# Kernel tuning notes

Hardware: AMD Instinct MI355X
Metric: run time of the kernel (lower is better)

## Reference

```python
import jax, jax.numpy as jnp
import numpy as np

D_MODEL = 768
N_HEADS = 12
HEAD_DIM = D_MODEL // N_HEADS


def setup_inputs() -> dict:
    key = jax.random.key(0)
    k1, k2, k3 = jax.random.split(key, 3)
    scale = 1.0 / np.sqrt(D_MODEL)
    x = jax.random.normal(k1, (2, 4096, D_MODEL), dtype=jnp.float32)
    W_qkv = jax.random.normal(k2, (D_MODEL, 3 * D_MODEL), dtype=jnp.float32) * scale
    b_qkv = jnp.zeros((3 * D_MODEL,), dtype=jnp.float32)
    W_out = jax.random.normal(k3, (D_MODEL, D_MODEL), dtype=jnp.float32) * scale
    b_out = jnp.zeros((D_MODEL,), dtype=jnp.float32)
    return {"x": x, "W_qkv": W_qkv, "b_qkv": b_qkv, "W_out": W_out, "b_out": b_out}


def reference(x, W_qkv, b_qkv, W_out, b_out):
    B, N, _ = x.shape
    # QKV projection: [B, N, 3*D]
    qkv = x @ W_qkv + b_qkv
    qkv = qkv.reshape(B, N, 3, N_HEADS, HEAD_DIM)
    qkv = jnp.transpose(qkv, (2, 0, 3, 1, 4))  # [3, B, H, N, Dh]
    q, k, v = qkv[0], qkv[1], qkv[2]
    # full NxN score matrix (faithful to the manual implementation)
    score = jnp.einsum('bhqd,bhkd->bhqk', q, k) / np.sqrt(HEAD_DIM).astype(np.float32)
    attn = jax.nn.softmax(score, axis=-1)
    out = jnp.einsum('bhqk,bhkd->bhqd', attn, v)  # [B, H, N, Dh]
    out = jnp.transpose(out, (0, 2, 1, 3)).reshape(B, N, D_MODEL)
    return out @ W_out + b_out
```

## Files before the change

kernel.cpp:

```cpp
#include <hip/hip_runtime.h>

typedef float  f32x4 __attribute__((ext_vector_type(4)));
typedef short  s16x8 __attribute__((ext_vector_type(8)));

__device__ __forceinline__ unsigned short f2bf(float f){
  unsigned int u = __builtin_bit_cast(unsigned int, f);
  return (unsigned short)((u + 0x8000u) >> 16);
}

__device__ __forceinline__ void mfma_bf16(f32x4& c, s16x8 a, s16x8 b){
  asm volatile("v_mfma_f32_16x16x32_bf16 %0, %1, %2, %0" : "+v"(c) : "v"(a), "v"(b));
}

__device__ __forceinline__ void split2(float x, unsigned short& h, unsigned short& l){
  unsigned int u = __builtin_bit_cast(unsigned int, x);
  h = (unsigned short)(u >> 16);
  float hf = __builtin_bit_cast(float, u & 0xFFFF0000u);
  l = (unsigned short)(__builtin_bit_cast(unsigned int, x - hf) >> 16);
}

__device__ __forceinline__ void pack16(const unsigned short* h, uint4& v0, uint4& v1){
  v0.x = h[0] | (h[1] << 16);  v0.y = h[2]  | (h[3] << 16);
  v0.z = h[4] | (h[5] << 16);  v0.w = h[6]  | (h[7] << 16);
  v1.x = h[8] | (h[9] << 16);  v1.y = h[10] | (h[11] << 16);
  v1.z = h[12]| (h[13]<< 16);  v1.w = h[14] | (h[15] << 16);
}

__global__ __launch_bounds__(256) void split_wT(
    const float* __restrict__ W, unsigned short* __restrict__ H,
    unsigned short* __restrict__ L, int N){
  __shared__ float T[64][69];
  const int t = threadIdx.x;
  const int n0 = blockIdx.x * 64, k0 = blockIdx.y * 64;
  {
    int kr = t >> 2, cg = (t & 3) * 16;
    const float* sp = &W[(size_t)(k0 + kr) * N + n0 + cg];
    #pragma unroll
    for (int q = 0; q < 4; ++q)
      *(float4*)&T[kr][cg + q*4] = *(const float4*)(sp + q*4);
  }
  __syncthreads();
  int nr = t >> 2, kg = (t & 3) * 16;
  unsigned short h[16], l[16];
  #pragma unroll
  for (int j = 0; j < 16; ++j) split2(T[kg + j][nr], h[j], l[j]);
  uint4 hv0, hv1, lv0, lv1;
  pack16(h, hv0, hv1);
  pack16(l, lv0, lv1);
  unsigned short* hp = &H[(size_t)(n0 + nr) * 768 + k0 + kg];
  unsigned short* lp = &L[(size_t)(n0 + nr) * 768 + k0 + kg];
  *(uint4*)hp = hv0; *(uint4*)(hp + 8) = hv1;
  *(uint4*)lp = lv0; *(uint4*)(lp + 8) = lv1;
}

__global__ __launch_bounds__(256) void qkv_mfma(
    const float* __restrict__ X,
    const unsigned short* __restrict__ WH, const unsigned short* __restrict__ WL,
    const float* __restrict__ bias, unsigned short* __restrict__ QKV){
  __shared__ __align__(16) char raw[36864];
  char* Abase = raw;
  char* Bbase = raw + 16384;
  const int tid = threadIdx.x;
  const int wave = tid >> 6, lane = tid & 63, r = lane & 15, g = lane >> 4;
  const int wm = wave >> 1, wn = wave & 1;
  const int m0 = blockIdx.y * 128, n0 = blockIdx.x * 128;
  const int srow = tid >> 1, shalf = tid & 1;
  const int sw  = (srow & 7) << 4;
  const int rsw = (r & 7) << 4;

  f32x4 acc[4][4] = {};

  for (int k0 = 0; k0 < 768; k0 += 32){
    const float* ax = &X[(size_t)(m0 + srow) * 768 + k0 + shalf * 16];
    float4 a0 = *(const float4*)ax,     a1 = *(const float4*)(ax + 4);
    float4 a2 = *(const float4*)(ax+8), a3 = *(const float4*)(ax + 12);
    float va[16] = {a0.x,a0.y,a0.z,a0.w, a1.x,a1.y,a1.z,a1.w,
                    a2.x,a2.y,a2.z,a2.w, a3.x,a3.y,a3.z,a3.w};
    unsigned short ah[16], al[16];
    #pragma unroll
    for (int j = 0; j < 16; ++j) split2(va[j], ah[j], al[j]);
    uint4 ah0, ah1, al0, al1;
    pack16(ah, ah0, ah1);
    pack16(al, al0, al1);
    const unsigned short* bwh = &WH[(size_t)(n0 + srow) * 768 + k0 + shalf * 16];
    const unsigned short* bwl = &WL[(size_t)(n0 + srow) * 768 + k0 + shalf * 16];
    uint4 bh0 = *(const uint4*)bwh, bh1 = *(const uint4*)(bwh + 8);
    uint4 bl0 = *(const uint4*)bwl, bl1 = *(const uint4*)(bwl + 8);
    __syncthreads();
    {
      char* ar = Abase + srow * 128;
      *(uint4*)(ar + ((shalf*32     ) ^ sw)) = ah0;
      *(uint4*)(ar + ((shalf*32 + 16) ^ sw)) = ah1;
      *(uint4*)(ar + ((64 + shalf*32     ) ^ sw)) = al0;
      *(uint4*)(ar + ((64 + shalf*32 + 16) ^ sw)) = al1;
      char* br = Bbase + srow * 128;
      *(uint4*)(br + ((shalf*32     ) ^ sw)) = bh0;
      *(uint4*)(br + ((shalf*32 + 16) ^ sw)) = bh1;
      *(uint4*)(br + ((64 + shalf*32     ) ^ sw)) = bl0;
      *(uint4*)(br + ((64 + shalf*32 + 16) ^ sw)) = bl1;
    }
    __syncthreads();
    s16x8 afh[4], afl[4], bfh[4], bfl[4];
    #pragma unroll
    for (int mf = 0; mf < 4; ++mf){
      char* p = Abase + (wm*64 + mf*16 + r) * 128;
      afh[mf] = *(const s16x8*)(p + ((g*16) ^ rsw));
      afl[mf] = *(const s16x8*)(p + ((64 + g*16) ^ rsw));
    }
    #pragma unroll
    for (int nf = 0; nf < 4; ++nf){
      char* p = Bbase + (wn*64 + nf*16 + r) * 128;
      bfh[nf] = *(const s16x8*)(p + ((g*16) ^ rsw));
      bfl[nf] = *(const s16x8*)(p + ((64 + g*16) ^ rsw));
    }
    #pragma unroll
    for (int mf = 0; mf < 4; ++mf)
      #pragma unroll
      for (int nf = 0; nf < 4; ++nf){
        mfma_bf16(acc[mf][nf], afh[mf], bfh[nf]);
        mfma_bf16(acc[mf][nf], afh[mf], bfl[nf]);
        mfma_bf16(acc[mf][nf], afl[mf], bfh[nf]);
      }
  }
  asm volatile("s_nop 7\n\ts_nop 7");
  __syncthreads();

  unsigned short (*ep)[72] = (unsigned short(*)[72])(raw + wave * 9216);
  const int ng0 = n0 + wn * 64;
  const int t3 = ng0 / 768, h = (ng0 % 768) / 64;
  const float sc = (t3 == 0) ? 0.18033688f : 1.0f;
  float bv[4];
  #pragma unroll
  for (int nf = 0; nf < 4; ++nf) bv[nf] = bias[ng0 + nf*16 + r];
  #pragma unroll
  for (int mf = 0; mf < 4; ++mf)
    #pragma unroll
    for (int nf = 0; nf < 4; ++nf)
      #pragma unroll
      for (int t = 0; t < 4; ++t)
        ep[mf*16 + g*4 + t][nf*16 + r] = f2bf((acc[mf][nf][t] + bv[nf]) * sc);
  __syncthreads();

  const int mg0 = m0 + wm * 64;
  const int bb = mg0 >> 12, nr0 = mg0 & 4095;
  unsigned short* dst = QKV + ((size_t)(bb*12 + h)*3 + t3) * 262144;
  if (t3 != 2){
    const int i0 = lane >> 3, ch = lane & 7;
    #pragma unroll
    for (int pass = 0; pass < 8; ++pass){
      int i = pass*8 + i0;
      *(uint4*)&dst[(size_t)(nr0 + i)*64 + ch*8] = *(const uint4*)&ep[i][ch*8];
    }
  } else {
    const int d0 = lane >> 3, kc = lane & 7;
    #pragma unroll
    for (int pass = 0; pass < 8; ++pass){
      int dh = pass*8 + d0;
      unsigned short v[8];
      #pragma unroll
      for (int j = 0; j < 8; ++j) v[j] = ep[kc*8 + j][dh];
      uint4 w;
      w.x = v[0] | (v[1] << 16); w.y = v[2] | (v[3] << 16);
      w.z = v[4] | (v[5] << 16); w.w = v[6] | (v[7] << 16);
      *(uint4*)&dst[(size_t)dh*4096 + nr0 + kc*8] = w;
    }
  }
}

__global__ __launch_bounds__(256, 3) void attn_kernel(
    const unsigned short* __restrict__ QKV, float* __restrict__ AO){
  __shared__ __align__(16) char lds[34816];
  char* Kt = lds;
  char* Vt = lds + 8192;
  const int tid  = threadIdx.x;
  const int wave = tid >> 6, lane = tid & 63;
  const int r = lane & 15, g = lane >> 4;
  const int rsw = (r & 7) << 4;
  unsigned short* pw = (unsigned short*)(lds + 16384 + wave * 4608);
  const int head = blockIdx.x % 24;
  const int qb   = blockIdx.x / 24;
  const size_t base = (size_t)head * 786432;
  const unsigned short* Q  = QKV + base;
  const unsigned short* K  = QKV + base + 262144;
  const unsigned short* VT = QKV + base + 524288;
  const int q0 = qb * 128 + wave * 32;

  s16x8 aq[2][2];
  #pragma unroll
  for (int qs = 0; qs < 2; ++qs){
    const unsigned short* qp = &Q[(size_t)(q0 + qs*16 + r)*64 + g*8];
    aq[qs][0] = *(const s16x8*)qp;
    aq[qs][1] = *(const s16x8*)(qp + 32);
  }

  const int c0 = wave*2, c1 = wave*2 + 1;
  const int srow = lane >> 3;
  const int scol = (lane & 7) * 8;
  const int sgr  = ((lane & 7) ^ srow) * 16;
  const int sdst0 = (c0*8 + srow) * 128 + sgr;
  const int sdst1 = (c1*8 + srow) * 128 + sgr;
  const unsigned short* Kg0 = K  + (size_t)(c0*8 + srow)*64 + scol;
  const unsigned short* Kg1 = K  + (size_t)(c1*8 + srow)*64 + scol;
  const unsigned short* Vg0 = VT + (size_t)(c0*8 + srow)*4096 + scol;
  const unsigned short* Vg1 = VT + (size_t)(c1*8 + srow)*4096 + scol;

  f32x4 o[2][4] = {};
  float lper[2][4] = {};
  uint4 kr0, kr1, vr0, vr1;

  kr0 = *(const uint4*)(Kg0);  kr1 = *(const uint4*)(Kg1);
  vr0 = *(const uint4*)(Vg0);  vr1 = *(const uint4*)(Vg1);
  *(uint4*)(Kt + sdst0) = kr0; *(uint4*)(Kt + sdst1) = kr1;
  *(uint4*)(Vt + sdst0) = vr0; *(uint4*)(Vt + sdst1) = vr1;
  __syncthreads();

  for (int it = 0; it < 64; ++it){
    const int kb = it * 64;
    if (it < 63){
      kr0 = *(const uint4*)(Kg0 + (size_t)(kb + 64)*64);
      kr1 = *(const uint4*)(Kg1 + (size_t)(kb + 64)*64);
      vr0 = *(const uint4*)(Vg0 + kb + 64);
      vr1 = *(const uint4*)(Vg1 + kb + 64);
    }
    f32x4 s[2][4];
    #pragma unroll
    for (int qs = 0; qs < 2; ++qs)
      #pragma unroll
      for (int kh = 0; kh < 4; ++kh) s[qs][kh] = (f32x4){0.f,0.f,0.f,0.f};
    #pragma unroll
    for (int kh = 0; kh < 4; ++kh){
      const char* kp = Kt + (kh*16 + r) * 128;
      s16x8 b0 = *(const s16x8*)(kp + ((g*16) ^ rsw));
      s16x8 b1 = *(const s16x8*)(kp + ((64 + g*16) ^ rsw));
      mfma_bf16(s[0][kh], aq[0][0], b0);
      mfma_bf16(s[0][kh], aq[0][1], b1);
      mfma_bf16(s[1][kh], aq[1][0], b0);
      mfma_bf16(s[1][kh], aq[1][1], b1);
    }
    asm volatile("s_nop 7\n\ts_nop 7");
    __builtin_amdgcn_sched_barrier(0);

    #pragma unroll
    for (int qs = 0; qs < 2; ++qs){
      #pragma unroll
      for (int t = 0; t < 4; ++t){
        float p0 = __builtin_amdgcn_exp2f(s[qs][0][t] - 16.0f);
        float p1 = __builtin_amdgcn_exp2f(s[qs][1][t] - 16.0f);
        float p2 = __builtin_amdgcn_exp2f(s[qs][2][t] - 16.0f);
        float p3 = __builtin_amdgcn_exp2f(s[qs][3][t] - 16.0f);
        lper[qs][t] += (p0 + p1) + (p2 + p3);
        unsigned short* row = pw + (qs*16 + g*4 + t)*72 + r;
        row[0]  = f2bf(p0);
        row[16] = f2bf(p1);
        row[32] = f2bf(p2);
        row[48] = f2bf(p3);
      }
    }

    s16x8 pf[2][2];
    #pragma unroll
    for (int qs = 0; qs < 2; ++qs){
      const unsigned short* pr = pw + (qs*16 + r)*72 + g*8;
      pf[qs][0] = *(const s16x8*)pr;
      pf[qs][1] = *(const s16x8*)(pr + 32);
    }
    #pragma unroll
    for (int dt = 0; dt < 4; ++dt){
      const char* vp = Vt + (dt*16 + r) * 128;
      s16x8 v0 = *(const s16x8*)(vp + ((g*16) ^ rsw));
      s16x8 v1 = *(const s16x8*)(vp + ((64 + g*16) ^ rsw));
      mfma_bf16(o[0][dt], pf[0][0], v0);
      mfma_bf16(o[0][dt], pf[0][1], v1);
      mfma_bf16(o[1][dt], pf[1][0], v0);
      mfma_bf16(o[1][dt], pf[1][1], v1);
    }

    if (it < 63){
      __syncthreads();
      *(uint4*)(Kt + sdst0) = kr0; *(uint4*)(Kt + sdst1) = kr1;
      *(uint4*)(Vt + sdst0) = vr0; *(uint4*)(Vt + sdst1) = vr1;
      __syncthreads();
    }
  }
  asm volatile("s_nop 7\n\ts_nop 7");
  __builtin_amdgcn_sched_barrier(0);

  const int bb = head / 12, h = head % 12;
  #pragma unroll
  for (int qs = 0; qs < 2; ++qs)
    #pragma unroll
    for (int t = 0; t < 4; ++t){
      float l = lper[qs][t];
      l += __shfl_xor(l, 1);
      l += __shfl_xor(l, 2);
      l += __shfl_xor(l, 4);
      l += __shfl_xor(l, 8);
      float inv = 1.0f / l;
      int q = q0 + qs*16 + g*4 + t;
      #pragma unroll
      for (int dt = 0; dt < 4; ++dt)
        AO[(size_t)(bb*4096 + q)*768 + h*64 + dt*16 + r] = o[qs][dt][t] * inv;
    }
}

__global__ __launch_bounds__(256) void out_mfma(
    const float* __restrict__ A,
    const unsigned short* __restrict__ WH, const unsigned short* __restrict__ WL,
    const float* __restrict__ bias, float* __restrict__ OUT){
  __shared__ __align__(16) char raw[32768];
  char* Abase = raw;
  char* Bbase = raw + 16384;
  const int tid = threadIdx.x;
  const int wave = tid >> 6, lane = tid & 63, r = lane & 15, g = lane >> 4;
  const int wm = wave >> 1, wn = wave & 1;
  const int m0 = blockIdx.y * 128, n0 = blockIdx.x * 128;
  const int srow = tid >> 1, shalf = tid & 1;
  const int sw  = (srow & 7) << 4;
  const int rsw = (r & 7) << 4;

  f32x4 acc[4][4] = {};

  for (int k0 = 0; k0 < 768; k0 += 32){
    const float* ax = &A[(size_t)(m0 + srow) * 768 + k0 + shalf * 16];
    float4 a0 = *(const float4*)ax,     a1 = *(const float4*)(ax + 4);
    float4 a2 = *(const float4*)(ax+8), a3 = *(const float4*)(ax + 12);
    float va[16] = {a0.x,a0.y,a0.z,a0.w, a1.x,a1.y,a1.z,a1.w,
                    a2.x,a2.y,a2.z,a2.w, a3.x,a3.y,a3.z,a3.w};
    unsigned short ah[16], al[16];
    #pragma unroll
    for (int j = 0; j < 16; ++j) split2(va[j], ah[j], al[j]);
    uint4 ah0, ah1, al0, al1;
    pack16(ah, ah0, ah1);
    pack16(al, al0, al1);
    const unsigned short* bwh = &WH[(size_t)(n0 + srow) * 768 + k0 + shalf * 16];
    const unsigned short* bwl = &WL[(size_t)(n0 + srow) * 768 + k0 + shalf * 16];
    uint4 bh0 = *(const uint4*)bwh, bh1 = *(const uint4*)(bwh + 8);
    uint4 bl0 = *(const uint4*)bwl, bl1 = *(const uint4*)(bwl + 8);
    __syncthreads();
    {
      char* ar = Abase + srow * 128;
      *(uint4*)(ar + ((shalf*32     ) ^ sw)) = ah0;
      *(uint4*)(ar + ((shalf*32 + 16) ^ sw)) = ah1;
      *(uint4*)(ar + ((64 + shalf*32     ) ^ sw)) = al0;
      *(uint4*)(ar + ((64 + shalf*32 + 16) ^ sw)) = al1;
      char* br = Bbase + srow * 128;
      *(uint4*)(br + ((shalf*32     ) ^ sw)) = bh0;
      *(uint4*)(br + ((shalf*32 + 16) ^ sw)) = bh1;
      *(uint4*)(br + ((64 + shalf*32     ) ^ sw)) = bl0;
      *(uint4*)(br + ((64 + shalf*32 + 16) ^ sw)) = bl1;
    }
    __syncthreads();
    s16x8 afh[4], afl[4], bfh[4], bfl[4];
    #pragma unroll
    for (int mf = 0; mf < 4; ++mf){
      char* p = Abase + (wm*64 + mf*16 + r) * 128;
      afh[mf] = *(const s16x8*)(p + ((g*16) ^ rsw));
      afl[mf] = *(const s16x8*)(p + ((64 + g*16) ^ rsw));
    }
    #pragma unroll
    for (int nf = 0; nf < 4; ++nf){
      char* p = Bbase + (wn*64 + nf*16 + r) * 128;
      bfh[nf] = *(const s16x8*)(p + ((g*16) ^ rsw));
      bfl[nf] = *(const s16x8*)(p + ((64 + g*16) ^ rsw));
    }
    #pragma unroll
    for (int mf = 0; mf < 4; ++mf)
      #pragma unroll
      for (int nf = 0; nf < 4; ++nf){
        mfma_bf16(acc[mf][nf], afh[mf], bfh[nf]);
        mfma_bf16(acc[mf][nf], afh[mf], bfl[nf]);
        mfma_bf16(acc[mf][nf], afl[mf], bfh[nf]);
      }
  }
  asm volatile("s_nop 7\n\ts_nop 7");
  __builtin_amdgcn_sched_barrier(0);

  #pragma unroll
  for (int nf = 0; nf < 4; ++nf){
    int n = n0 + wn*64 + nf*16 + r;
    float bv = bias[n];
    #pragma unroll
    for (int mf = 0; mf < 4; ++mf)
      #pragma unroll
      for (int t = 0; t < 4; ++t)
        OUT[(size_t)(m0 + wm*64 + mf*16 + g*4 + t)*768 + n] = acc[mf][nf][t] + bv;
  }
}

extern "C" void kernel_launch(void* const* d_in, const int* in_sizes, int n_in,
                              void* d_out, int out_size, void* d_ws, size_t ws_size,
                              hipStream_t stream){
  const float* x    = (const float*)d_in[0];
  const float* Wqkv = (const float*)d_in[1];
  const float* bqkv = (const float*)d_in[2];
  const float* Wout = (const float*)d_in[3];
  const float* bout = (const float*)d_in[4];
  float* out = (float*)d_out;

  char* ws = (char*)d_ws;
  unsigned short* qkv  = (unsigned short*)ws;
  unsigned short* wqth = (unsigned short*)(ws + 37748736);
  unsigned short* wqtl = (unsigned short*)(ws + 41287680);
  float*          ao   = (float*)         (ws + 37748736);
  unsigned short* woth = (unsigned short*)ws;
  unsigned short* wotl = (unsigned short*)(ws + 1179648);

  split_wT <<<dim3(36, 12), 256, 0, stream>>>(Wqkv, wqth, wqtl, 2304);
  qkv_mfma <<<dim3(18, 64), 256, 0, stream>>>(x, wqth, wqtl, bqkv, qkv);
  attn_kernel<<<768, 256, 0, stream>>>(qkv, ao);
  split_wT <<<dim3(12, 12), 256, 0, stream>>>(Wout, woth, wotl, 768);
  out_mfma <<<dim3(6, 64), 256, 0, stream>>>(ao, woth, wotl, bout, out);
}
```

Measured before the change: 365.8 us.

## Keep P in registers via transposed QK^T and presplit X/attn-out into bf16 hi/lo

The attention kernel now computes S^T (K as the A operand), so the exp'd probabilities already sit in the MFMA A-operand layout. They are packed with v_cvt_pk_bf16_f32 straight into registers instead of round-tripping through LDS, and V is stored with a permuted LDS layout to match. The row-sum reduction is simplified. X is split into bf16 hi/lo once by a new split_x kernel, using the output buffer as scratch. Attention writes its output already split into hi/lo bf16, so both GEMMs skip the per-tile conversion at the cost of an extra launch and different V store patterns.

```diff
diff --git a/kernel.cpp b/kernel.cpp
--- a/kernel.cpp
+++ b/kernel.cpp
@@ -24,6 +24,25 @@
   v0.z = h[4] | (h[5] << 16);  v0.w = h[6]  | (h[7] << 16);
   v1.x = h[8] | (h[9] << 16);  v1.y = h[10] | (h[11] << 16);
   v1.z = h[12]| (h[13]<< 16);  v1.w = h[14] | (h[15] << 16);
+}
+
+__global__ __launch_bounds__(256) void split_x(
+    const float* __restrict__ X, unsigned short* __restrict__ H,
+    unsigned short* __restrict__ L){
+  int i = blockIdx.x * 256 + threadIdx.x;
+  const float4* p = (const float4*)(X + (size_t)i * 8);
+  float4 a = p[0], b = p[1];
+  float v[8] = {a.x, a.y, a.z, a.w, b.x, b.y, b.z, b.w};
+  unsigned short h[8], l[8];
+  #pragma unroll
+  for (int jj = 0; jj < 8; ++jj) split2(v[jj], h[jj], l[jj]);
+  uint4 hv, lv;
+  hv.x = h[0] | (h[1] << 16); hv.y = h[2] | (h[3] << 16);
+  hv.z = h[4] | (h[5] << 16); hv.w = h[6] | (h[7] << 16);
+  lv.x = l[0] | (l[1] << 16); lv.y = l[2] | (l[3] << 16);
+  lv.z = l[4] | (l[5] << 16); lv.w = l[6] | (l[7] << 16);
+  *(uint4*)(H + (size_t)i * 8) = hv;
+  *(uint4*)(L + (size_t)i * 8) = lv;
 }
 
 __global__ __launch_bounds__(256) void split_wT(
@@ -43,7 +62,7 @@
   int nr = t >> 2, kg = (t & 3) * 16;
   unsigned short h[16], l[16];
   #pragma unroll
-  for (int j = 0; j < 16; ++j) split2(T[kg + j][nr], h[j], l[j]);
+  for (int jj = 0; jj < 16; ++jj) split2(T[kg + jj][nr], h[jj], l[jj]);
   uint4 hv0, hv1, lv0, lv1;
   pack16(h, hv0, hv1);
   pack16(l, lv0, lv1);
@@ -54,7 +73,7 @@
 }
 
 __global__ __launch_bounds__(256) void qkv_mfma(
-    const float* __restrict__ X,
+    const unsigned short* __restrict__ XH, const unsigned short* __restrict__ XL,
     const unsigned short* __restrict__ WH, const unsigned short* __restrict__ WL,
     const float* __restrict__ bias, unsigned short* __restrict__ QKV){
   __shared__ __align__(16) char raw[36864];
@@ -71,17 +90,10 @@
   f32x4 acc[4][4] = {};
 
   for (int k0 = 0; k0 < 768; k0 += 32){
-    const float* ax = &X[(size_t)(m0 + srow) * 768 + k0 + shalf * 16];
-    float4 a0 = *(const float4*)ax,     a1 = *(const float4*)(ax + 4);
-    float4 a2 = *(const float4*)(ax+8), a3 = *(const float4*)(ax + 12);
-    float va[16] = {a0.x,a0.y,a0.z,a0.w, a1.x,a1.y,a1.z,a1.w,
-                    a2.x,a2.y,a2.z,a2.w, a3.x,a3.y,a3.z,a3.w};
-    unsigned short ah[16], al[16];
-    #pragma unroll
-    for (int j = 0; j < 16; ++j) split2(va[j], ah[j], al[j]);
-    uint4 ah0, ah1, al0, al1;
-    pack16(ah, ah0, ah1);
-    pack16(al, al0, al1);
+    const unsigned short* axh = &XH[(size_t)(m0 + srow) * 768 + k0 + shalf * 16];
+    const unsigned short* axl = &XL[(size_t)(m0 + srow) * 768 + k0 + shalf * 16];
+    uint4 ah0 = *(const uint4*)axh, ah1 = *(const uint4*)(axh + 8);
+    uint4 al0 = *(const uint4*)axl, al1 = *(const uint4*)(axl + 8);
     const unsigned short* bwh = &WH[(size_t)(n0 + srow) * 768 + k0 + shalf * 16];
     const unsigned short* bwl = &WL[(size_t)(n0 + srow) * 768 + k0 + shalf * 16];
     uint4 bh0 = *(const uint4*)bwh, bh1 = *(const uint4*)(bwh + 8);
@@ -158,7 +170,7 @@
       int dh = pass*8 + d0;
       unsigned short v[8];
       #pragma unroll
-      for (int j = 0; j < 8; ++j) v[j] = ep[kc*8 + j][dh];
+      for (int jj = 0; jj < 8; ++jj) v[jj] = ep[kc*8 + jj][dh];
       uint4 w;
       w.x = v[0] | (v[1] << 16); w.y = v[2] | (v[3] << 16);
       w.z = v[4] | (v[5] << 16); w.w = v[6] | (v[7] << 16);
@@ -168,15 +180,15 @@
 }
 
 __global__ __launch_bounds__(256, 3) void attn_kernel(
-    const unsigned short* __restrict__ QKV, float* __restrict__ AO){
-  __shared__ __align__(16) char lds[34816];
+    const unsigned short* __restrict__ QKV,
+    unsigned short* __restrict__ AOH, unsigned short* __restrict__ AOL){
+  __shared__ __align__(16) char lds[16384];
   char* Kt = lds;
   char* Vt = lds + 8192;
   const int tid  = threadIdx.x;
   const int wave = tid >> 6, lane = tid & 63;
   const int r = lane & 15, g = lane >> 4;
   const int rsw = (r & 7) << 4;
-  unsigned short* pw = (unsigned short*)(lds + 16384 + wave * 4608);
   const int head = blockIdx.x % 24;
   const int qb   = blockIdx.x / 24;
   const size_t base = (size_t)head * 786432;
@@ -194,24 +206,33 @@
   }
 
   const int c0 = wave*2, c1 = wave*2 + 1;
-  const int srow = lane >> 3;
-  const int scol = (lane & 7) * 8;
-  const int sgr  = ((lane & 7) ^ srow) * 16;
-  const int sdst0 = (c0*8 + srow) * 128 + sgr;
-  const int sdst1 = (c1*8 + srow) * 128 + sgr;
+  const int srow = (lane >> 3) & 7;
+  const int j    = lane & 7;
+  const int scol = j * 8;
+  const int kdst0 = (c0*8 + srow)*128 + ((j ^ srow) << 4);
+  const int kdst1 = (c1*8 + srow)*128 + ((j ^ srow) << 4);
+  const int X   = 64*(j>>2) + 32*(j&1) + 8*((j>>1)&1);
+  const int swb = srow << 4;
+  const int vA0 = (c0*8 + srow)*128 + ( X       ^ swb);
+  const int vA1 = (c0*8 + srow)*128 + ((X + 16) ^ swb);
+  const int vB0 = (c1*8 + srow)*128 + ( X       ^ swb);
+  const int vB1 = (c1*8 + srow)*128 + ((X + 16) ^ swb);
   const unsigned short* Kg0 = K  + (size_t)(c0*8 + srow)*64 + scol;
   const unsigned short* Kg1 = K  + (size_t)(c1*8 + srow)*64 + scol;
   const unsigned short* Vg0 = VT + (size_t)(c0*8 + srow)*4096 + scol;
   const unsigned short* Vg1 = VT + (size_t)(c1*8 + srow)*4096 + scol;
 
   f32x4 o[2][4] = {};
-  float lper[2][4] = {};
+  float lper[2] = {0.f, 0.f};
   uint4 kr0, kr1, vr0, vr1;
 
   kr0 = *(const uint4*)(Kg0);  kr1 = *(const uint4*)(Kg1);
   vr0 = *(const uint4*)(Vg0);  vr1 = *(const uint4*)(Vg1);
-  *(uint4*)(Kt + sdst0) = kr0; *(uint4*)(Kt + sdst1) = kr1;
-  *(uint4*)(Vt + sdst0) = vr0; *(uint4*)(Vt + sdst1) = vr1;
+  *(uint4*)(Kt + kdst0) = kr0; *(uint4*)(Kt + kdst1) = kr1;
+  *(uint2*)(Vt + vA0) = make_uint2(vr0.x, vr0.y);
+  *(uint2*)(Vt + vA1) = make_uint2(vr0.z, vr0.w);
+  *(uint2*)(Vt + vB0) = make_uint2(vr1.x, vr1.y);
+  *(uint2*)(Vt + vB1) = make_uint2(vr1.z, vr1.w);
   __syncthreads();
 
   for (int it = 0; it < 64; ++it){
@@ -222,63 +243,68 @@
       vr0 = *(const uint4*)(Vg0 + kb + 64);
       vr1 = *(const uint4*)(Vg1 + kb + 64);
     }
-    f32x4 s[2][4];
-    #pragma unroll
-    for (int qs = 0; qs < 2; ++qs)
-      #pragma unroll
-      for (int kh = 0; kh < 4; ++kh) s[qs][kh] = (f32x4){0.f,0.f,0.f,0.f};
-    #pragma unroll
-    for (int kh = 0; kh < 4; ++kh){
-      const char* kp = Kt + (kh*16 + r) * 128;
-      s16x8 b0 = *(const s16x8*)(kp + ((g*16) ^ rsw));
-      s16x8 b1 = *(const s16x8*)(kp + ((64 + g*16) ^ rsw));
-      mfma_bf16(s[0][kh], aq[0][0], b0);
-      mfma_bf16(s[0][kh], aq[0][1], b1);
-      mfma_bf16(s[1][kh], aq[1][0], b0);
-      mfma_bf16(s[1][kh], aq[1][1], b1);
+    f32x4 c[4][2];
+    #pragma unroll
+    for (int kt = 0; kt < 4; ++kt)
+      #pragma unroll
+      for (int qt = 0; qt < 2; ++qt) c[kt][qt] = (f32x4){0.f,0.f,0.f,0.f};
+    #pragma unroll
+    for (int kt = 0; kt < 4; ++kt){
+      const char* kp = Kt + (kt*16 + r) * 128;
+      s16x8 kf0 = *(const s16x8*)(kp + ((g*16) ^ rsw));
+      s16x8 kf1 = *(const s16x8*)(kp + ((64 + g*16) ^ rsw));
+      mfma_bf16(c[kt][0], kf0, aq[0][0]);
+      mfma_bf16(c[kt][0], kf1, aq[0][1]);
+      mfma_bf16(c[kt][1], kf0, aq[1][0]);
+      mfma_bf16(c[kt][1], kf1, aq[1][1]);
     }
     asm volatile("s_nop 7\n\ts_nop 7");
     __builtin_amdgcn_sched_barrier(0);
 
-    #pragma unroll
-    for (int qs = 0; qs < 2; ++qs){
-      #pragma unroll
-      for (int t = 0; t < 4; ++t){
-        float p0 = __builtin_amdgcn_exp2f(s[qs][0][t] - 16.0f);
-        float p1 = __builtin_amdgcn_exp2f(s[qs][1][t] - 16.0f);
-        float p2 = __builtin_amdgcn_exp2f(s[qs][2][t] - 16.0f);
-        float p3 = __builtin_amdgcn_exp2f(s[qs][3][t] - 16.0f);
-        lper[qs][t] += (p0 + p1) + (p2 + p3);
-        unsigned short* row = pw + (qs*16 + g*4 + t)*72 + r;
-        row[0]  = f2bf(p0);
-        row[16] = f2bf(p1);
-        row[32] = f2bf(p2);
-        row[48] = f2bf(p3);
+    s16x8 pa[2][2];
+    #pragma unroll
+    for (int qt = 0; qt < 2; ++qt){
+      float pp[4][4];
+      float ls = 0.f;
+      #pragma unroll
+      for (int kt = 0; kt < 4; ++kt)
+        #pragma unroll
+        for (int t = 0; t < 4; ++t){
+          float pv = __builtin_amdgcn_exp2f(c[kt][qt][t] - 16.0f);
+          pp[kt][t] = pv; ls += pv;
+        }
+      lper[qt] += ls;
+      #pragma unroll
+      for (int H = 0; H < 2; ++H){
+        unsigned int w0, w1, w2, w3;
+        asm("v_cvt_pk_bf16_f32 %0, %1, %2" : "=v"(w0) : "v"(pp[2*H][0]),   "v"(pp[2*H][1]));
+        asm("v_cvt_pk_bf16_f32 %0, %1, %2" : "=v"(w1) : "v"(pp[2*H][2]),   "v"(pp[2*H][3]));
+        asm("v_cvt_pk_bf16_f32 %0, %1, %2" : "=v"(w2) : "v"(pp[2*H+1][0]), "v"(pp[2*H+1][1]));
+        asm("v_cvt_pk_bf16_f32 %0, %1, %2" : "=v"(w3) : "v"(pp[2*H+1][2]), "v"(pp[2*H+1][3]));
+        uint4 wv; wv.x = w0; wv.y = w1; wv.z = w2; wv.w = w3;
+        pa[qt][H] = __builtin_bit_cast(s16x8, wv);
       }
     }
-
-    s16x8 pf[2][2];
-    #pragma unroll
-    for (int qs = 0; qs < 2; ++qs){
-      const unsigned short* pr = pw + (qs*16 + r)*72 + g*8;
-      pf[qs][0] = *(const s16x8*)pr;
-      pf[qs][1] = *(const s16x8*)(pr + 32);
-    }
+    asm volatile("s_nop 3");
+
     #pragma unroll
     for (int dt = 0; dt < 4; ++dt){
       const char* vp = Vt + (dt*16 + r) * 128;
-      s16x8 v0 = *(const s16x8*)(vp + ((g*16) ^ rsw));
-      s16x8 v1 = *(const s16x8*)(vp + ((64 + g*16) ^ rsw));
-      mfma_bf16(o[0][dt], pf[0][0], v0);
-      mfma_bf16(o[0][dt], pf[0][1], v1);
-      mfma_bf16(o[1][dt], pf[1][0], v0);
-      mfma_bf16(o[1][dt], pf[1][1], v1);
+      s16x8 vf0 = *(const s16x8*)(vp + ((g*16) ^ rsw));
+      s16x8 vf1 = *(const s16x8*)(vp + ((64 + g*16) ^ rsw));
+      mfma_bf16(o[0][dt], pa[0][0], vf0);
+      mfma_bf16(o[0][dt], pa[0][1], vf1);
+      mfma_bf16(o[1][dt], pa[1][0], vf0);
+      mfma_bf16(o[1][dt], pa[1][1], vf1);
     }
 
     if (it < 63){
       __syncthreads();
-      *(uint4*)(Kt + sdst0) = kr0; *(uint4*)(Kt + sdst1) = kr1;
-      *(uint4*)(Vt + sdst0) = vr0; *(uint4*)(Vt + sdst1) = vr1;
+      *(uint4*)(Kt + kdst0) = kr0; *(uint4*)(Kt + kdst1) = kr1;
+      *(uint2*)(Vt + vA0) = make_uint2(vr0.x, vr0.y);
+      *(uint2*)(Vt + vA1) = make_uint2(vr0.z, vr0.w);
+      *(uint2*)(Vt + vB0) = make_uint2(vr1.x, vr1.y);
+      *(uint2*)(Vt + vB1) = make_uint2(vr1.z, vr1.w);
       __syncthreads();
     }
   }
@@ -286,25 +312,33 @@
   __builtin_amdgcn_sched_barrier(0);
 
   const int bb = head / 12, h = head % 12;
-  #pragma unroll
-  for (int qs = 0; qs < 2; ++qs)
+  float inv[2];
+  #pragma unroll
+  for (int qt = 0; qt < 2; ++qt){
+    float l = lper[qt];
+    l += __shfl_xor(l, 16);
+    l += __shfl_xor(l, 32);
+    inv[qt] = 1.0f / l;
+  }
+  #pragma unroll
+  for (int qt = 0; qt < 2; ++qt)
     #pragma unroll
     for (int t = 0; t < 4; ++t){
-      float l = lper[qs][t];
-      l += __shfl_xor(l, 1);
-      l += __shfl_xor(l, 2);
-      l += __shfl_xor(l, 4);
-      l += __shfl_xor(l, 8);
-      float inv = 1.0f / l;
-      int q = q0 + qs*16 + g*4 + t;
-      #pragma unroll
-      for (int dt = 0; dt < 4; ++dt)
-        AO[(size_t)(bb*4096 + q)*768 + h*64 + dt*16 + r] = o[qs][dt][t] * inv;
+      float iv = __shfl(inv[qt], g*4 + t);
+      int q = q0 + qt*16 + g*4 + t;
+      #pragma unroll
+      for (int dt = 0; dt < 4; ++dt){
+        float val = o[qt][dt][t] * iv;
+        unsigned short hh, ll;
+        split2(val, hh, ll);
+        size_t idx = (size_t)(bb*4096 + q)*768 + h*64 + dt*16 + r;
+        AOH[idx] = hh; AOL[idx] = ll;
+      }
     }
 }
 
 __global__ __launch_bounds__(256) void out_mfma(
-    const float* __restrict__ A,
+    const unsigned short* __restrict__ AH, const unsigned short* __restrict__ AL,
     const unsigned short* __restrict__ WH, const unsigned short* __restrict__ WL,
     const float* __restrict__ bias, float* __restrict__ OUT){
   __shared__ __align__(16) char raw[32768];
@@ -321,17 +355,10 @@
   f32x4 acc[4][4] = {};
 
   for (int k0 = 0; k0 < 768; k0 += 32){
-    const float* ax = &A[(size_t)(m0 + srow) * 768 + k0 + shalf * 16];
-    float4 a0 = *(const float4*)ax,     a1 = *(const float4*)(ax + 4);
-    float4 a2 = *(const float4*)(ax+8), a3 = *(const float4*)(ax + 12);
-    float va[16] = {a0.x,a0.y,a0.z,a0.w, a1.x,a1.y,a1.z,a1.w,
-                    a2.x,a2.y,a2.z,a2.w, a3.x,a3.y,a3.z,a3.w};
-    unsigned short ah[16], al[16];
-    #pragma unroll
-    for (int j = 0; j < 16; ++j) split2(va[j], ah[j], al[j]);
-    uint4 ah0, ah1, al0, al1;
-    pack16(ah, ah0, ah1);
-    pack16(al, al0, al1);
+    const unsigned short* axh = &AH[(size_t)(m0 + srow) * 768 + k0 + shalf * 16];
+    const unsigned short* axl = &AL[(size_t)(m0 + srow) * 768 + k0 + shalf * 16];
+    uint4 ah0 = *(const uint4*)axh, ah1 = *(const uint4*)(axh + 8);
+    uint4 al0 = *(const uint4*)axl, al1 = *(const uint4*)(axl + 8);
     const unsigned short* bwh = &WH[(size_t)(n0 + srow) * 768 + k0 + shalf * 16];
     const unsigned short* bwl = &WL[(size_t)(n0 + srow) * 768 + k0 + shalf * 16];
     uint4 bh0 = *(const uint4*)bwh, bh1 = *(const uint4*)(bwh + 8);
@@ -398,16 +425,20 @@
   float* out = (float*)d_out;
 
   char* ws = (char*)d_ws;
+  unsigned short* xh   = (unsigned short*)d_out;
+  unsigned short* xl   = xh + 6291456;
   unsigned short* qkv  = (unsigned short*)ws;
   unsigned short* wqth = (unsigned short*)(ws + 37748736);
   unsigned short* wqtl = (unsigned short*)(ws + 41287680);
-  float*          ao   = (float*)         (ws + 37748736);
+  unsigned short* aoh  = (unsigned short*)(ws + 37748736);
+  unsigned short* aol  = (unsigned short*)(ws + 50331648);
   unsigned short* woth = (unsigned short*)ws;
   unsigned short* wotl = (unsigned short*)(ws + 1179648);
 
+  split_x  <<<3072, 256, 0, stream>>>(x, xh, xl);
   split_wT <<<dim3(36, 12), 256, 0, stream>>>(Wqkv, wqth, wqtl, 2304);
-  qkv_mfma <<<dim3(18, 64), 256, 0, stream>>>(x, wqth, wqtl, bqkv, qkv);
-  attn_kernel<<<768, 256, 0, stream>>>(qkv, ao);
+  qkv_mfma <<<dim3(18, 64), 256, 0, stream>>>(xh, xl, wqth, wqtl, bqkv, qkv);
+  attn_kernel<<<768, 256, 0, stream>>>(qkv, aoh, aol);
   split_wT <<<dim3(12, 12), 256, 0, stream>>>(Wout, woth, wotl, 768);
-  out_mfma <<<dim3(6, 64), 256, 0, stream>>>(ao, woth, wotl, bout, out);
-}
+  out_mfma <<<dim3(6, 64), 256, 0, stream>>>(aoh, aol, woth, wotl, bout, out);
+}
```

Result: faster. 350.0 us (-4.3%).
